# Kernel optimization log

Hardware: AMD Instinct MI355X
Metric: run time of the kernel (lower is better)

Reference implementation:

```python
import jax, jax.numpy as jnp
import numpy as np

# Graph geometry: G complete graphs (molecules) of n nodes each.
N_PER_G, G, DEG = 64, 256, 16
H, D = 8, 8
IN_DIM = H * D      # 64
EDGE_DIM = 64
N = N_PER_G * G                      # 16384 nodes
EF = G * N_PER_G * N_PER_G           # 1,048,576 full edges
ES = G * N_PER_G * DEG               # 262,144 sparse edges
SCALE = float(np.sqrt(D))


def _edges():
    n = N_PER_G
    # full graph: all (i -> j) pairs per block, edge id = b*n*n + i*n + j
    ij = np.arange(n * n)
    i, j = ij // n, ij % n
    b = np.arange(G)[:, None]
    src_full = (b * n + i[None, :]).reshape(-1).astype(np.int32)
    dst_full = (b * n + j[None, :]).reshape(-1).astype(np.int32)
    # sparse graph: each dst j receives from DEG distinct sources (j+1..j+DEG mod n)
    jj = np.arange(n)[:, None]
    kk = np.arange(DEG)[None, :]
    ii = (jj + 1 + kk) % n
    eid_block = (ii * n + jj).reshape(-1)                 # [n*DEG]
    sparse_eid = (np.arange(G)[:, None] * n * n + eid_block[None, :]).reshape(-1).astype(np.int32)
    return jnp.asarray(src_full), jnp.asarray(dst_full), jnp.asarray(sparse_eid)


def setup_inputs() -> dict:
    key = jax.random.key(0)
    ks = jax.random.split(key, 16)
    w = lambda k, shape, s=0.05: s * jax.random.normal(k, shape, jnp.float32)
    src_full, dst_full, sparse_eid = _edges()
    return dict(
        h=jax.random.normal(ks[0], (N, IN_DIM), jnp.float32),
        e=jax.random.normal(ks[1], (ES, EDGE_DIM), jnp.float32),
        adj2=jax.random.uniform(ks[2], (EF,), jnp.float32),
        rel_pos_3d=jax.random.normal(ks[3], (EF, H), jnp.float32),
        Wq=w(ks[4], (H * D, IN_DIM)), bq=jnp.zeros((H * D,), jnp.float32),
        Wk=w(ks[5], (H * D, IN_DIM)), bk=jnp.zeros((H * D,), jnp.float32),
        Wv=w(ks[6], (H * D, IN_DIM)), bv=jnp.zeros((H * D,), jnp.float32),
        Wpe=w(ks[7], (H, EDGE_DIM)), bpe=jnp.zeros((H,), jnp.float32),
        Wap=w(ks[8], (EDGE_DIM, H)), bap=jnp.zeros((EDGE_DIM,), jnp.float32),
        Wo=w(ks[9], (H * D, H * D)), bo=jnp.zeros((H * D,), jnp.float32),
        Woe=w(ks[10], (EDGE_DIM, EDGE_DIM)), boe=jnp.zeros((EDGE_DIM,), jnp.float32),
        src_full=src_full, dst_full=dst_full, sparse_eid=sparse_eid,
    )


def reference(h, e, adj2, rel_pos_3d, Wq, bq, Wk, bk, Wv, bv, Wpe, bpe,
              Wap, bap, Wo, bo, Woe, boe, src_full, dst_full, sparse_eid):
    Qh = (h @ Wq.T + bq).reshape(N, H, D)
    Kh = (h @ Wk.T + bk).reshape(N, H, D)
    Vh = (h @ Wv.T + bv).reshape(N, H, D)
    proj_e = e @ Wpe.T + bpe                                   # [ES, H]
    # edge-wise QK dot (src=K, dst=Q), scaled, then gaussian-decay + rel-pos bias
    score = jnp.sum(Kh[src_full] * Qh[dst_full], axis=-1) / SCALE   # [EF, H]
    score = score * adj2[:, None] + rel_pos_3d                      # [EF, H]
    # gather sparse-subgraph scores, project for edge output, add proj_e bias
    sc_sp = score[sparse_eid]                                        # [ES, H]
    e_out_raw = sc_sp @ Wap.T + bap                                  # [ES, EDGE_DIM]
    score = score.at[sparse_eid].set(sc_sp + proj_e)
    # edge softmax over incoming edges of each destination node
    logits = jnp.clip(score, -5.0, 5.0)
    m = jax.ops.segment_max(logits, dst_full, num_segments=N)
    ex = jnp.exp(logits - m[dst_full])
    den = jax.ops.segment_sum(ex, dst_full, num_segments=N)
    attn = ex / den[dst_full]                                        # [EF, H]
    # weighted scatter-sum of source values
    wV = jax.ops.segment_sum(Vh[src_full] * attn[..., None], dst_full, num_segments=N)
    h_out = wV.reshape(N, H * D) @ Wo.T + bo
    e_out = (e_out_raw + e) @ Woe.T + boe
    return h_out, e_out
```

## Files before the change

kernel.cpp:

```cpp
#include <hip/hip_runtime.h>


__global__ __launch_bounds__(512, 2) void qkvpe_kernel(
    const float* __restrict__ h,
    const float* __restrict__ e,
    const float* __restrict__ Wq, const float* __restrict__ bq,
    const float* __restrict__ Wk, const float* __restrict__ bk,
    const float* __restrict__ Wv, const float* __restrict__ bv,
    const float* __restrict__ Wpe, const float* __restrict__ bpe,
    float* __restrict__ Qs, float* __restrict__ Ks, float* __restrict__ Vs,
    float* __restrict__ PEs)
{
    const int t = threadIdx.x;
    if (blockIdx.x < 256) {
        const int b    = blockIdx.x;
        const int lane = t & 63;
        const int wu   = __builtin_amdgcn_readfirstlane(t >> 6);
        const float* hrow = h + (size_t)(b * 64 + lane) * 64;
        float accQ[8], accK[8], accV[8];
        #pragma unroll
        for (int cc = 0; cc < 8; ++cc) {
            const int c = wu * 8 + cc;
            accQ[cc] = bq[c]; accK[cc] = bk[c]; accV[cc] = bv[c];
        }
        #pragma unroll 1
        for (int k0 = 0; k0 < 4; ++k0) {
            float hv[16];
            #pragma unroll
            for (int u = 0; u < 4; ++u) {
                const float4 x = ((const float4*)hrow)[k0 * 4 + u];
                hv[u*4+0] = x.x; hv[u*4+1] = x.y; hv[u*4+2] = x.z; hv[u*4+3] = x.w;
            }
            #pragma unroll
            for (int cc = 0; cc < 8; ++cc) {
                const int c = wu * 8 + cc;
                const float* wq  = Wq + c * 64 + k0 * 16;
                const float* wk  = Wk + c * 64 + k0 * 16;
                const float* wvp = Wv + c * 64 + k0 * 16;
                #pragma unroll
                for (int k = 0; k < 16; ++k) {
                    accQ[cc] = fmaf(hv[k], wq[k],  accQ[cc]);
                    accK[cc] = fmaf(hv[k], wk[k],  accK[cc]);
                    accV[cc] = fmaf(hv[k], wvp[k], accV[cc]);
                }
            }
        }
        const size_t o = (size_t)(b * 64 + lane) * 64 + wu * 8;
        *(float4*)(Qs + o)     = make_float4(accQ[0], accQ[1], accQ[2], accQ[3]);
        *(float4*)(Qs + o + 4) = make_float4(accQ[4], accQ[5], accQ[6], accQ[7]);
        *(float4*)(Ks + o)     = make_float4(accK[0], accK[1], accK[2], accK[3]);
        *(float4*)(Ks + o + 4) = make_float4(accK[4], accK[5], accK[6], accK[7]);
        *(float4*)(Vs + o)     = make_float4(accV[0], accV[1], accV[2], accV[3]);
        *(float4*)(Vs + o + 4) = make_float4(accV[4], accV[5], accV[6], accV[7]);
    } else {
        const int row = (blockIdx.x - 256) * 512 + t;
        const float* erow = e + (size_t)row * 64;
        float acc[8];
        #pragma unroll
        for (int h2 = 0; h2 < 8; ++h2) acc[h2] = bpe[h2];
        #pragma unroll 1
        for (int k0 = 0; k0 < 4; ++k0) {
            float ev[16];
            #pragma unroll
            for (int u = 0; u < 4; ++u) {
                const float4 x = ((const float4*)erow)[k0 * 4 + u];
                ev[u*4+0] = x.x; ev[u*4+1] = x.y; ev[u*4+2] = x.z; ev[u*4+3] = x.w;
            }
            #pragma unroll
            for (int h2 = 0; h2 < 8; ++h2) {
                const float* wp = Wpe + h2 * 64 + k0 * 16;
                #pragma unroll
                for (int k = 0; k < 16; ++k)
                    acc[h2] = fmaf(ev[k], wp[k], acc[h2]);
            }
        }
        float* p0 = PEs + (size_t)row * 8;
        *(float4*)(p0)     = make_float4(acc[0], acc[1], acc[2], acc[3]);
        *(float4*)(p0 + 4) = make_float4(acc[4], acc[5], acc[6], acc[7]);
    }
}

#define STAGE_RELADJ(c4_) {                                                   \
    const int il_ = t >> 6;                                                   \
    *(float4*)&shRel[il_ * 264 + (t & 63) * 4] =                              \
        *(const float4*)(relBase + ((c4_) * 16 + il_) * 512 + (t & 63) * 4);  \
    if (t < 512) {                                                            \
        const int ia_ = t >> 5, jl_ = t & 31;                                 \
        shAdj[ia_ * 36 + jl_] = adjBase[((c4_) * 16 + ia_) * 64 + jl_];       \
    } }

__global__ __launch_bounds__(1024, 2) void attn_kernel(
    const float* __restrict__ Qs, const float* __restrict__ Ks,
    const float* __restrict__ Vs, const float* __restrict__ PEs,
    const float* __restrict__ adj2,
    const float* __restrict__ rel,
    const float* __restrict__ Wo, const float* __restrict__ bo,
    float* __restrict__ h_out,
    float* __restrict__ scsp)
{
    __shared__ float shK[64 * 64];
    __shared__ float shV[64 * 64];
    __shared__ float shPE[512 * 8];
    __shared__ float shRel[16 * 264];
    __shared__ float shAdj[16 * 36];

    const int b2   = blockIdx.x;
    const int b    = b2 >> 1;
    const int joff = (b2 & 1) << 5;
    const int t    = threadIdx.x;

    const int j_local = t >> 5;
    const int hh      = (t >> 2) & 7;
    const int q4      = t & 3;
    const int j       = joff + j_local;

    const float* relBase = rel  + (size_t)b * 32768 + joff * 8;
    const float* adjBase = adj2 + (size_t)b * 4096  + joff;

    {
        const int r  = t >> 4;
        const int gh = t & 15;
        const int g  = gh >> 1, lo = (gh & 1) * 4;
        const int d  = r * 64 + ((g ^ (r & 7)) << 3) + lo;
        const int so = r * 64 + g * 8 + lo;
        shK[d + 0] = Ks[(size_t)b * 4096 + so + 0];
        shK[d + 1] = Ks[(size_t)b * 4096 + so + 1];
        shK[d + 2] = Ks[(size_t)b * 4096 + so + 2];
        shK[d + 3] = Ks[(size_t)b * 4096 + so + 3];
        shV[d + 0] = Vs[(size_t)b * 4096 + so + 0];
        shV[d + 1] = Vs[(size_t)b * 4096 + so + 1];
        shV[d + 2] = Vs[(size_t)b * 4096 + so + 2];
        shV[d + 3] = Vs[(size_t)b * 4096 + so + 3];
        *(float4*)&shPE[t * 4] =
            *(const float4*)(PEs + ((size_t)b * 1024 + joff * 16) * 8 + t * 4);
    }
    STAGE_RELADJ(0);
    float q[8];
    {
        const float* qp = Qs + (size_t)(b * 64 + j) * 64 + hh * 8;
        const float4 a = *(const float4*)qp;
        const float4 c = *(const float4*)(qp + 4);
        q[0]=a.x; q[1]=a.y; q[2]=a.z; q[3]=a.w;
        q[4]=c.x; q[5]=c.y; q[6]=c.z; q[7]=c.w;
    }

    float den = 0.f;
    float wv[8] = {0.f,0.f,0.f,0.f,0.f,0.f,0.f,0.f};
    const float inv_scale = 0.35355339059327379f;
    #pragma unroll 1
    for (int c4 = 0; c4 < 4; ++c4) {
        __syncthreads();
        #pragma unroll
        for (int it2 = 0; it2 < 4; ++it2) {
            const int il = it2 * 4 + q4;
            const int i  = c4 * 16 + il;
            const float a2 = shAdj[il * 36 + j_local];
            const float rp = shRel[il * 264 + j_local * 8 + hh];
            const int kb = i * 64 + ((hh ^ (i & 7)) << 3);
            const float4 kA = *(const float4*)&shK[kb];
            const float4 kB = *(const float4*)&shK[kb + 4];
            float s;
            s = kA.x * q[0];
            s = fmaf(kA.y, q[1], s); s = fmaf(kA.z, q[2], s); s = fmaf(kA.w, q[3], s);
            s = fmaf(kB.x, q[4], s); s = fmaf(kB.y, q[5], s); s = fmaf(kB.z, q[6], s);
            s = fmaf(kB.w, q[7], s);
            s = fmaf(s * inv_scale, a2, rp);
            const int kidx = (i - j - 1) & 63;
            if (kidx < 16) {
                const int x = (j_local * 16 + kidx) * 8 + hh;
                const float pe = shPE[x];
                shPE[x] = s;
                s += pe;
            }
            s = fminf(fmaxf(s, -5.f), 5.f);
            const float ex = __expf(s);
            den += ex;
            const float4 vA = *(const float4*)&shV[kb];
            const float4 vB = *(const float4*)&shV[kb + 4];
            wv[0] = fmaf(ex, vA.x, wv[0]); wv[1] = fmaf(ex, vA.y, wv[1]);
            wv[2] = fmaf(ex, vA.z, wv[2]); wv[3] = fmaf(ex, vA.w, wv[3]);
            wv[4] = fmaf(ex, vB.x, wv[4]); wv[5] = fmaf(ex, vB.y, wv[5]);
            wv[6] = fmaf(ex, vB.z, wv[6]); wv[7] = fmaf(ex, vB.w, wv[7]);
        }
        if (c4 < 3) {
            __syncthreads();
            STAGE_RELADJ(c4 + 1);
        }
    }
    den += __shfl_xor(den, 1);
    den += __shfl_xor(den, 2);
    #pragma unroll
    for (int u = 0; u < 8; ++u) {
        wv[u] += __shfl_xor(wv[u], 1);
        wv[u] += __shfl_xor(wv[u], 2);
    }
    __syncthreads();

    {
        const int row = t >> 1, pp = t & 1;
        *(float4*)(scsp + (size_t)((size_t)b * 1024 + joff * 16 + row) * 8 + pp * 4) =
            *(const float4*)&shPE[row * 8 + pp * 4];
    }
    if (q4 == 0) {
        const float id = 1.f / den;
        float* wp = &shK[j_local * 64 + hh * 8];
        *(float4*)(wp)     = make_float4(wv[0]*id, wv[1]*id, wv[2]*id, wv[3]*id);
        *(float4*)(wp + 4) = make_float4(wv[4]*id, wv[5]*id, wv[6]*id, wv[7]*id);
    }
    __syncthreads();

    {
        const int rl = t >> 5;
        const int c0 = (t & 31) * 2;
        float acc[2];
        acc[0] = bo[c0]; acc[1] = bo[c0 + 1];
        #pragma unroll 1
        for (int k0 = 0; k0 < 4; ++k0) {
            float tv[16];
            #pragma unroll
            for (int u = 0; u < 4; ++u) {
                const float4 x = *(const float4*)&shK[rl * 64 + k0 * 16 + u * 4];
                tv[u*4+0] = x.x; tv[u*4+1] = x.y; tv[u*4+2] = x.z; tv[u*4+3] = x.w;
            }
            #pragma unroll
            for (int u = 0; u < 2; ++u) {
                const float* wo = Wo + (c0 + u) * 64 + k0 * 16;
                #pragma unroll
                for (int k = 0; k < 16; ++k)
                    acc[u] = fmaf(tv[k], wo[k], acc[u]);
            }
        }
        float* orow = h_out + (size_t)(b * 64 + joff + rl) * 64 + c0;
        *(float2*)orow = make_float2(acc[0], acc[1]);
    }
}

__global__ void prep_kernel(const float* __restrict__ Wap, const float* __restrict__ bap,
                            const float* __restrict__ Woe, const float* __restrict__ boe,
                            float* __restrict__ M2, float* __restrict__ Tm, int hasT)
{
    const int tg = blockIdx.x * 64 + threadIdx.x;
    if (tg < 512) {
        const int c = tg >> 3, hq = tg & 7;
        float s = 0.f;
        #pragma unroll 8
        for (int k = 0; k < 64; ++k) s = fmaf(Woe[c * 64 + k], Wap[k * 8 + hq], s);
        M2[tg] = s;
    } else if (tg < 576) {
        const int c = tg - 512;
        float s = boe[c];
        #pragma unroll 8
        for (int k = 0; k < 64; ++k) s = fmaf(bap[k], Woe[c * 64 + k], s);
        M2[512 + c] = s;
    } else if (hasT && tg < 576 + 73 * 64) {
        const int idx = tg - 576;
        const int k = idx >> 6, c = idx & 63;
        float v;
        if (k < 64) {
            v = Woe[c * 64 + k];
        } else if (k < 72) {
            const int hq = k - 64;
            v = 0.f;
            #pragma unroll 8
            for (int kk = 0; kk < 64; ++kk)
                v = fmaf(Woe[c * 64 + kk], Wap[kk * 8 + hq], v);
        } else {
            v = boe[c];
            #pragma unroll 8
            for (int kk = 0; kk < 64; ++kk)
                v = fmaf(bap[kk], Woe[c * 64 + kk], v);
        }
        Tm[k * 64 + c] = v;
    }
}

__global__ __launch_bounds__(256, 2) void eoutT_kernel(
    const float* __restrict__ e,
    const float* __restrict__ scsp,
    const float* __restrict__ Tm,
    float* __restrict__ e_out)
{
    __shared__ float shET[64 * 67];
    __shared__ float shS[64 * 8];

    const int t    = threadIdx.x;
    const int base = blockIdx.x * 64;

    {
        const int r0 = t >> 2, qq = t & 3;
        const float* ep = e + (size_t)(base + r0) * 64 + qq * 16;
        #pragma unroll
        for (int v = 0; v < 4; ++v) {
            const float4 x = ((const float4*)ep)[v];
            const int c = qq * 16 + v * 4;
            shET[(c + 0) * 67 + r0] = x.x;
            shET[(c + 1) * 67 + r0] = x.y;
            shET[(c + 2) * 67 + r0] = x.z;
            shET[(c + 3) * 67 + r0] = x.w;
        }
    }
    if (t < 128) {
        const int r = t >> 1, pp = t & 1;
        *(float4*)&shS[r * 8 + pp * 4] =
            *(const float4*)(scsp + (size_t)(base + r) * 8 + pp * 4);
    }
    __syncthreads();

    const int w = __builtin_amdgcn_readfirstlane(t >> 6);
    const int r = t & 63;

    float sc[8];
    {
        const float4 a  = *(const float4*)&shS[r * 8];
        const float4 c4 = *(const float4*)&shS[r * 8 + 4];
        sc[0]=a.x; sc[1]=a.y; sc[2]=a.z; sc[3]=a.w;
        sc[4]=c4.x; sc[5]=c4.y; sc[6]=c4.z; sc[7]=c4.w;
    }
    float acc[16];
    {
        const float* bcw = Tm + 72 * 64 + w * 16;
        #pragma unroll
        for (int u = 0; u < 16; ++u) acc[u] = bcw[u];
    }
    #pragma unroll
    for (int k = 0; k < 64; ++k) {
        const float evk = shET[k * 67 + r];
        const float* wk = Tm + k * 64 + w * 16;
        #pragma unroll
        for (int u = 0; u < 16; ++u)
            acc[u] = fmaf(evk, wk[u], acc[u]);
    }
    #pragma unroll
    for (int hq = 0; hq < 8; ++hq) {
        const float* wk = Tm + (64 + hq) * 64 + w * 16;
        #pragma unroll
        for (int u = 0; u < 16; ++u)
            acc[u] = fmaf(sc[hq], wk[u], acc[u]);
    }
    float* orow = e_out + (size_t)(base + r) * 64 + w * 16;
    #pragma unroll
    for (int u = 0; u < 4; ++u)
        *(float4*)&orow[u * 4] =
            make_float4(acc[u*4+0], acc[u*4+1], acc[u*4+2], acc[u*4+3]);
}

__global__ __launch_bounds__(256, 2) void eout_kernel(
    const float* __restrict__ e,
    const float* __restrict__ scsp,
    const float* __restrict__ Woe,
    const float* __restrict__ M2g,
    float* __restrict__ e_out)
{
    __shared__ float shE[64 * 64];
    __shared__ float shS[64 * 8];
    const int t    = threadIdx.x;
    const int base = blockIdx.x * 64;
    {
        const int r = t >> 2, qq = t & 3;
        const float* ep = e + (size_t)(base + r) * 64 + qq * 16;
        #pragma unroll
        for (int u = 0; u < 4; ++u) {
            const float4 x = ((const float4*)ep)[u];
            const int cc = qq * 4 + u;
            *(float4*)&shE[r * 64 + ((cc ^ (r & 15)) << 2)] = x;
        }
    }
    if (t < 128) {
        const int r = t >> 1, pp = t & 1;
        *(float4*)&shS[r * 8 + pp * 4] =
            *(const float4*)(scsp + (size_t)(base + r) * 8 + pp * 4);
    }
    __syncthreads();
    const int w = __builtin_amdgcn_readfirstlane(t >> 6);
    const int r = t & 63;
    float sc[8];
    {
        const float4 a  = *(const float4*)&shS[r * 8];
        const float4 c4 = *(const float4*)&shS[r * 8 + 4];
        sc[0]=a.x; sc[1]=a.y; sc[2]=a.z; sc[3]=a.w;
        sc[4]=c4.x; sc[5]=c4.y; sc[6]=c4.z; sc[7]=c4.w;
    }
    float acc[16];
    #pragma unroll
    for (int u = 0; u < 16; ++u) {
        const int c = w * 16 + u;
        float s = M2g[512 + c];
        #pragma unroll
        for (int hq = 0; hq < 8; ++hq)
            s = fmaf(sc[hq], M2g[c * 8 + hq], s);
        acc[u] = s;
    }
    #pragma unroll
    for (int k0 = 0; k0 < 4; ++k0) {
        float ev[16];
        #pragma unroll
        for (int v = 0; v < 4; ++v) {
            const int cc = k0 * 4 + v;
            const float4 x = *(const float4*)&shE[r * 64 + ((cc ^ (r & 15)) << 2)];
            ev[v*4+0] = x.x; ev[v*4+1] = x.y; ev[v*4+2] = x.z; ev[v*4+3] = x.w;
        }
        #pragma unroll
        for (int u = 0; u < 16; ++u) {
            const float* wr = Woe + (w * 16 + u) * 64 + k0 * 16;
            #pragma unroll
            for (int k = 0; k < 16; ++k)
                acc[u] = fmaf(ev[k], wr[k], acc[u]);
        }
    }
    float* orow = e_out + (size_t)(base + r) * 64 + w * 16;
    #pragma unroll
    for (int u = 0; u < 4; ++u)
        *(float4*)&orow[u * 4] =
            make_float4(acc[u*4+0], acc[u*4+1], acc[u*4+2], acc[u*4+3]);
}

extern "C" void kernel_launch(void* const* d_in, const int* in_sizes, int n_in,
                              void* d_out, int out_size, void* d_ws, size_t ws_size,
                              hipStream_t stream) {
    const float* h    = (const float*)d_in[0];
    const float* e    = (const float*)d_in[1];
    const float* adj2 = (const float*)d_in[2];
    const float* rel  = (const float*)d_in[3];
    const float* Wq   = (const float*)d_in[4];  const float* bq  = (const float*)d_in[5];
    const float* Wk   = (const float*)d_in[6];  const float* bk  = (const float*)d_in[7];
    const float* Wv   = (const float*)d_in[8];  const float* bv  = (const float*)d_in[9];
    const float* Wpe  = (const float*)d_in[10]; const float* bpe = (const float*)d_in[11];
    const float* Wap  = (const float*)d_in[12]; const float* bap = (const float*)d_in[13];
    const float* Wo   = (const float*)d_in[14]; const float* bo  = (const float*)d_in[15];
    const float* Woe  = (const float*)d_in[16]; const float* boe = (const float*)d_in[17];

    float* out  = (float*)d_out;
    float* hout = out;
    float* eout = out + 16384 * 64;
    float* Qs   = eout;
    float* Ks   = eout + 1048576;
    float* Vs   = eout + 2097152;
    float* PEs  = eout + 3145728;
    float* ws   = (float*)d_ws;
    float* scsp = ws;
    float* M2g  = ws + 2097152;
    float* Tm   = ws + 2098176;
    const int hasT = (ws_size >= (size_t)(2098176 + 73 * 64) * sizeof(float)) ? 1 : 0;

    prep_kernel<<<dim3(82), dim3(64), 0, stream>>>(Wap, bap, Woe, boe, M2g, Tm, hasT);
    qkvpe_kernel<<<dim3(768), dim3(512), 0, stream>>>(
        h, e, Wq, bq, Wk, bk, Wv, bv, Wpe, bpe, Qs, Ks, Vs, PEs);
    attn_kernel<<<dim3(512), dim3(1024), 0, stream>>>(
        Qs, Ks, Vs, PEs, adj2, rel, Wo, bo, hout, scsp);
    if (hasT)
        eoutT_kernel<<<dim3(4096), dim3(256), 0, stream>>>(e, scsp, Tm, eout);
    else
        eout_kernel<<<dim3(4096), dim3(256), 0, stream>>>(e, scsp, Woe, M2g, eout);
}
```

Baseline: 139.3 us.

## Remap attention threads over source chunks and register-tile the edge-output GEMM

The attention kernel now splits the 64 source nodes into four chunks handled by separate thread groups. It reads rel_pos and adj2 directly from global memory with coalesced per-(j,h) loads, which removes the staged LDS buffers and the per-chunk barriers; partial softmax sums are then combined through a serial shared-memory reduction. The eoutT kernel stages the combined Tm matrix in LDS, appends the sparse scores as extra rows of the transposed e tile, and computes a 4x4 register tile per thread over 72 k-steps. The intent is fewer barriers and more FMA per LDS load, at the cost of extra syncs in the reduction. The float4 LDS reads on a stride-69 layout may be misaligned.

```diff
diff --git a/kernel.cpp b/kernel.cpp
--- a/kernel.cpp
+++ b/kernel.cpp
@@ -80,15 +80,6 @@
     }
 }
 
-#define STAGE_RELADJ(c4_) {                                                   \
-    const int il_ = t >> 6;                                                   \
-    *(float4*)&shRel[il_ * 264 + (t & 63) * 4] =                              \
-        *(const float4*)(relBase + ((c4_) * 16 + il_) * 512 + (t & 63) * 4);  \
-    if (t < 512) {                                                            \
-        const int ia_ = t >> 5, jl_ = t & 31;                                 \
-        shAdj[ia_ * 36 + jl_] = adjBase[((c4_) * 16 + ia_) * 64 + jl_];       \
-    } }
-
 __global__ __launch_bounds__(1024, 2) void attn_kernel(
     const float* __restrict__ Qs, const float* __restrict__ Ks,
     const float* __restrict__ Vs, const float* __restrict__ PEs,
@@ -101,21 +92,17 @@
     __shared__ float shK[64 * 64];
     __shared__ float shV[64 * 64];
     __shared__ float shPE[512 * 8];
-    __shared__ float shRel[16 * 264];
-    __shared__ float shAdj[16 * 36];
+    __shared__ float shRed[256 * 9];
 
     const int b2   = blockIdx.x;
     const int b    = b2 >> 1;
     const int joff = (b2 & 1) << 5;
     const int t    = threadIdx.x;
 
-    const int j_local = t >> 5;
-    const int hh      = (t >> 2) & 7;
-    const int q4      = t & 3;
+    const int j_local = (t >> 3) & 31;
+    const int hh      = t & 7;
+    const int q4      = t >> 8;
     const int j       = joff + j_local;
-
-    const float* relBase = rel  + (size_t)b * 32768 + joff * 8;
-    const float* adjBase = adj2 + (size_t)b * 4096  + joff;
 
     {
         const int r  = t >> 4;
@@ -134,7 +121,6 @@
         *(float4*)&shPE[t * 4] =
             *(const float4*)(PEs + ((size_t)b * 1024 + joff * 16) * 8 + t * 4);
     }
-    STAGE_RELADJ(0);
     float q[8];
     {
         const float* qp = Qs + (size_t)(b * 64 + j) * 64 + hh * 8;
@@ -143,56 +129,67 @@
         q[0]=a.x; q[1]=a.y; q[2]=a.z; q[3]=a.w;
         q[4]=c.x; q[5]=c.y; q[6]=c.z; q[7]=c.w;
     }
+    __syncthreads();
 
     float den = 0.f;
     float wv[8] = {0.f,0.f,0.f,0.f,0.f,0.f,0.f,0.f};
+    const float* relP = rel  + (size_t)b * 32768 + (size_t)(joff + j_local) * 8 + hh;
+    const float* adjP = adj2 + (size_t)b * 4096 + j;
     const float inv_scale = 0.35355339059327379f;
-    #pragma unroll 1
-    for (int c4 = 0; c4 < 4; ++c4) {
-        __syncthreads();
-        #pragma unroll
-        for (int it2 = 0; it2 < 4; ++it2) {
-            const int il = it2 * 4 + q4;
-            const int i  = c4 * 16 + il;
-            const float a2 = shAdj[il * 36 + j_local];
-            const float rp = shRel[il * 264 + j_local * 8 + hh];
-            const int kb = i * 64 + ((hh ^ (i & 7)) << 3);
-            const float4 kA = *(const float4*)&shK[kb];
-            const float4 kB = *(const float4*)&shK[kb + 4];
-            float s;
-            s = kA.x * q[0];
-            s = fmaf(kA.y, q[1], s); s = fmaf(kA.z, q[2], s); s = fmaf(kA.w, q[3], s);
-            s = fmaf(kB.x, q[4], s); s = fmaf(kB.y, q[5], s); s = fmaf(kB.z, q[6], s);
-            s = fmaf(kB.w, q[7], s);
-            s = fmaf(s * inv_scale, a2, rp);
-            const int kidx = (i - j - 1) & 63;
-            if (kidx < 16) {
-                const int x = (j_local * 16 + kidx) * 8 + hh;
-                const float pe = shPE[x];
-                shPE[x] = s;
-                s += pe;
-            }
-            s = fminf(fmaxf(s, -5.f), 5.f);
-            const float ex = __expf(s);
-            den += ex;
-            const float4 vA = *(const float4*)&shV[kb];
-            const float4 vB = *(const float4*)&shV[kb + 4];
-            wv[0] = fmaf(ex, vA.x, wv[0]); wv[1] = fmaf(ex, vA.y, wv[1]);
-            wv[2] = fmaf(ex, vA.z, wv[2]); wv[3] = fmaf(ex, vA.w, wv[3]);
-            wv[4] = fmaf(ex, vB.x, wv[4]); wv[5] = fmaf(ex, vB.y, wv[5]);
-            wv[6] = fmaf(ex, vB.z, wv[6]); wv[7] = fmaf(ex, vB.w, wv[7]);
-        }
-        if (c4 < 3) {
-            __syncthreads();
-            STAGE_RELADJ(c4 + 1);
-        }
-    }
-    den += __shfl_xor(den, 1);
-    den += __shfl_xor(den, 2);
-    #pragma unroll
-    for (int u = 0; u < 8; ++u) {
-        wv[u] += __shfl_xor(wv[u], 1);
-        wv[u] += __shfl_xor(wv[u], 2);
+    #pragma unroll 4
+    for (int it = 0; it < 16; ++it) {
+        const int i  = (q4 << 4) + it;
+        const float rp = relP[(size_t)i * 512];
+        const float a2 = adjP[(size_t)i * 64];
+        const int kb = i * 64 + ((hh ^ (i & 7)) << 3);
+        const float4 kA = *(const float4*)&shK[kb];
+        const float4 kB = *(const float4*)&shK[kb + 4];
+        float s;
+        s = kA.x * q[0];
+        s = fmaf(kA.y, q[1], s); s = fmaf(kA.z, q[2], s); s = fmaf(kA.w, q[3], s);
+        s = fmaf(kB.x, q[4], s); s = fmaf(kB.y, q[5], s); s = fmaf(kB.z, q[6], s);
+        s = fmaf(kB.w, q[7], s);
+        s = fmaf(s * inv_scale, a2, rp);
+        const int kidx = (i - j - 1) & 63;
+        if (kidx < 16) {
+            const int x = (j_local * 16 + kidx) * 8 + hh;
+            const float pe = shPE[x];
+            shPE[x] = s;
+            s += pe;
+        }
+        s = fminf(fmaxf(s, -5.f), 5.f);
+        const float ex = __expf(s);
+        den += ex;
+        const float4 vA = *(const float4*)&shV[kb];
+        const float4 vB = *(const float4*)&shV[kb + 4];
+        wv[0] = fmaf(ex, vA.x, wv[0]); wv[1] = fmaf(ex, vA.y, wv[1]);
+        wv[2] = fmaf(ex, vA.z, wv[2]); wv[3] = fmaf(ex, vA.w, wv[3]);
+        wv[4] = fmaf(ex, vB.x, wv[4]); wv[5] = fmaf(ex, vB.y, wv[5]);
+        wv[6] = fmaf(ex, vB.z, wv[6]); wv[7] = fmaf(ex, vB.w, wv[7]);
+    }
+    const int jh = t & 255;
+    if (q4 == 0) {
+        #pragma unroll
+        for (int u = 0; u < 8; ++u) shRed[jh * 9 + u] = wv[u];
+        shRed[jh * 9 + 8] = den;
+    }
+    __syncthreads();
+    if (q4 == 1) {
+        #pragma unroll
+        for (int u = 0; u < 8; ++u) shRed[jh * 9 + u] += wv[u];
+        shRed[jh * 9 + 8] += den;
+    }
+    __syncthreads();
+    if (q4 == 2) {
+        #pragma unroll
+        for (int u = 0; u < 8; ++u) shRed[jh * 9 + u] += wv[u];
+        shRed[jh * 9 + 8] += den;
+    }
+    __syncthreads();
+    if (q4 == 3) {
+        #pragma unroll
+        for (int u = 0; u < 8; ++u) shRed[jh * 9 + u] += wv[u];
+        shRed[jh * 9 + 8] += den;
     }
     __syncthreads();
 
@@ -201,11 +198,12 @@
         *(float4*)(scsp + (size_t)((size_t)b * 1024 + joff * 16 + row) * 8 + pp * 4) =
             *(const float4*)&shPE[row * 8 + pp * 4];
     }
-    if (q4 == 0) {
-        const float id = 1.f / den;
-        float* wp = &shK[j_local * 64 + hh * 8];
-        *(float4*)(wp)     = make_float4(wv[0]*id, wv[1]*id, wv[2]*id, wv[3]*id);
-        *(float4*)(wp + 4) = make_float4(wv[4]*id, wv[5]*id, wv[6]*id, wv[7]*id);
+    if (t < 256) {
+        const float* rd = &shRed[t * 9];
+        const float id = 1.f / rd[8];
+        float* wp = &shK[(t >> 3) * 64 + (t & 7) * 8];
+        *(float4*)(wp)     = make_float4(rd[0]*id, rd[1]*id, rd[2]*id, rd[3]*id);
+        *(float4*)(wp + 4) = make_float4(rd[4]*id, rd[5]*id, rd[6]*id, rd[7]*id);
     }
     __syncthreads();
 
@@ -280,8 +278,8 @@
     const float* __restrict__ Tm,
     float* __restrict__ e_out)
 {
-    __shared__ float shET[64 * 67];
-    __shared__ float shS[64 * 8];
+    __shared__ float shET[72 * 69];
+    __shared__ float shTm[73 * 64];
 
     const int t    = threadIdx.x;
     const int base = blockIdx.x * 64;
@@ -293,55 +291,58 @@
         for (int v = 0; v < 4; ++v) {
             const float4 x = ((const float4*)ep)[v];
             const int c = qq * 16 + v * 4;
-            shET[(c + 0) * 67 + r0] = x.x;
-            shET[(c + 1) * 67 + r0] = x.y;
-            shET[(c + 2) * 67 + r0] = x.z;
-            shET[(c + 3) * 67 + r0] = x.w;
+            shET[(c + 0) * 69 + r0] = x.x;
+            shET[(c + 1) * 69 + r0] = x.y;
+            shET[(c + 2) * 69 + r0] = x.z;
+            shET[(c + 3) * 69 + r0] = x.w;
         }
     }
     if (t < 128) {
         const int r = t >> 1, pp = t & 1;
-        *(float4*)&shS[r * 8 + pp * 4] =
-            *(const float4*)(scsp + (size_t)(base + r) * 8 + pp * 4);
-    }
-    __syncthreads();
-
-    const int w = __builtin_amdgcn_readfirstlane(t >> 6);
-    const int r = t & 63;
-
-    float sc[8];
-    {
-        const float4 a  = *(const float4*)&shS[r * 8];
-        const float4 c4 = *(const float4*)&shS[r * 8 + 4];
-        sc[0]=a.x; sc[1]=a.y; sc[2]=a.z; sc[3]=a.w;
-        sc[4]=c4.x; sc[5]=c4.y; sc[6]=c4.z; sc[7]=c4.w;
-    }
+        const float4 s4 = *(const float4*)(scsp + (size_t)(base + r) * 8 + pp * 4);
+        shET[(64 + pp * 4 + 0) * 69 + r] = s4.x;
+        shET[(64 + pp * 4 + 1) * 69 + r] = s4.y;
+        shET[(64 + pp * 4 + 2) * 69 + r] = s4.z;
+        shET[(64 + pp * 4 + 3) * 69 + r] = s4.w;
+    }
+    #pragma unroll
+    for (int v = 0; v < 5; ++v) {
+        const int fi = v * 256 + t;
+        if (fi < 1168)
+            *(float4*)&shTm[fi * 4] = *(const float4*)(Tm + fi * 4);
+    }
+    __syncthreads();
+
+    const int rq = t >> 4;
+    const int cq = t & 15;
+
     float acc[16];
     {
-        const float* bcw = Tm + 72 * 64 + w * 16;
-        #pragma unroll
-        for (int u = 0; u < 16; ++u) acc[u] = bcw[u];
-    }
-    #pragma unroll
-    for (int k = 0; k < 64; ++k) {
-        const float evk = shET[k * 67 + r];
-        const float* wk = Tm + k * 64 + w * 16;
-        #pragma unroll
-        for (int u = 0; u < 16; ++u)
-            acc[u] = fmaf(evk, wk[u], acc[u]);
-    }
-    #pragma unroll
-    for (int hq = 0; hq < 8; ++hq) {
-        const float* wk = Tm + (64 + hq) * 64 + w * 16;
-        #pragma unroll
-        for (int u = 0; u < 16; ++u)
-            acc[u] = fmaf(sc[hq], wk[u], acc[u]);
-    }
-    float* orow = e_out + (size_t)(base + r) * 64 + w * 16;
-    #pragma unroll
-    for (int u = 0; u < 4; ++u)
-        *(float4*)&orow[u * 4] =
-            make_float4(acc[u*4+0], acc[u*4+1], acc[u*4+2], acc[u*4+3]);
+        const float4 bcv = *(const float4*)&shTm[72 * 64 + cq * 4];
+        #pragma unroll
+        for (int ri = 0; ri < 4; ++ri) {
+            acc[ri*4+0] = bcv.x; acc[ri*4+1] = bcv.y;
+            acc[ri*4+2] = bcv.z; acc[ri*4+3] = bcv.w;
+        }
+    }
+    #pragma unroll
+    for (int k = 0; k < 72; ++k) {
+        const float4 ev = *(const float4*)&shET[k * 69 + rq * 4];
+        const float4 wk = *(const float4*)&shTm[k * 64 + cq * 4];
+        acc[0]  = fmaf(ev.x, wk.x, acc[0]);  acc[1]  = fmaf(ev.x, wk.y, acc[1]);
+        acc[2]  = fmaf(ev.x, wk.z, acc[2]);  acc[3]  = fmaf(ev.x, wk.w, acc[3]);
+        acc[4]  = fmaf(ev.y, wk.x, acc[4]);  acc[5]  = fmaf(ev.y, wk.y, acc[5]);
+        acc[6]  = fmaf(ev.y, wk.z, acc[6]);  acc[7]  = fmaf(ev.y, wk.w, acc[7]);
+        acc[8]  = fmaf(ev.z, wk.x, acc[8]);  acc[9]  = fmaf(ev.z, wk.y, acc[9]);
+        acc[10] = fmaf(ev.z, wk.z, acc[10]); acc[11] = fmaf(ev.z, wk.w, acc[11]);
+        acc[12] = fmaf(ev.w, wk.x, acc[12]); acc[13] = fmaf(ev.w, wk.y, acc[13]);
+        acc[14] = fmaf(ev.w, wk.z, acc[14]); acc[15] = fmaf(ev.w, wk.w, acc[15]);
+    }
+    #pragma unroll
+    for (int ri = 0; ri < 4; ++ri) {
+        float* orow = e_out + (size_t)(base + rq * 4 + ri) * 64 + cq * 4;
+        *(float4*)orow = make_float4(acc[ri*4+0], acc[ri*4+1], acc[ri*4+2], acc[ri*4+3]);
+    }
 }
 
 __global__ __launch_bounds__(256, 2) void eout_kernel(
```

Measured after the change: 130.9 us. 6.0% less time.
